# Kernel optimization log

Hardware: AMD Instinct MI355X
Metric: run time of the kernel (lower is better)

## Reference

```python
import jax, jax.numpy as jnp
import numpy as np

NUM_HEADS = 8
KERNEL = 3


def _arsinh_norm(x, w, b):
    # ArsinhNorm with scale=1.0: weight * asinh(x) + bias
    return w * jnp.arcsinh(x) + b


def _nbr_idx(L, k):
    # NATTEN neighborhood: window start clamped so the k-window stays in-bounds
    start = jnp.clip(jnp.arange(L) - k // 2, 0, L - k)
    return start[:, None] + jnp.arange(k)  # [L, k]


def _na2d(x, qkv_w, qkv_b, proj_w, proj_b, num_heads=NUM_HEADS, k=KERNEL):
    B, H, W, C = x.shape
    hd = C // num_heads
    qkv = x @ qkv_w + qkv_b                      # [B,H,W,3C]
    q, kk, v = jnp.split(qkv, 3, axis=-1)
    q = q.reshape(B, H, W, num_heads, hd) * (hd ** -0.5)
    kk = kk.reshape(B, H, W, num_heads, hd)
    v = v.reshape(B, H, W, num_heads, hd)
    ri = _nbr_idx(H, k)[:, None, :, None]        # [H,1,k,1]
    ci = _nbr_idx(W, k)[None, :, None, :]        # [1,W,1,k]
    nb_k = kk[:, ri, ci].reshape(B, H, W, k * k, num_heads, hd)  # gather 3x3 neighborhood
    nb_v = v[:, ri, ci].reshape(B, H, W, k * k, num_heads, hd)
    scores = jnp.einsum('bijnd,bijmnd->bijnm', q, nb_k)          # [B,H,W,nh,k*k]
    attn = jax.nn.softmax(scores, axis=-1)
    out = jnp.einsum('bijnm,bijmnd->bijnd', attn, nb_v).reshape(B, H, W, C)
    return out @ proj_w + proj_b


def setup_inputs() -> dict:
    key = jax.random.key(0)
    ks = jax.random.split(key, 8)
    B, H, W, C = 16, 64, 64, 256
    s = 0.02
    return {
        'h': jax.random.normal(ks[0], (B, H, W, C), dtype=jnp.float32),
        'qkv_w': jax.random.normal(ks[1], (C, 3 * C), dtype=jnp.float32) * s,
        'qkv_b': jnp.zeros((3 * C,), jnp.float32),
        'proj_w': jax.random.normal(ks[2], (C, C), dtype=jnp.float32) * s,
        'proj_b': jnp.zeros((C,), jnp.float32),
        'n1_w': jnp.ones((C,), jnp.float32),
        'n1_b': jnp.zeros((C,), jnp.float32),
        'n2_w': jnp.ones((C,), jnp.float32),
        'n2_b': jnp.zeros((C,), jnp.float32),
        'mlp_w1': jax.random.normal(ks[3], (C, 2 * C), dtype=jnp.float32) * s,
        'mlp_b1': jnp.zeros((2 * C,), jnp.float32),
        'mlp_w2': jax.random.normal(ks[4], (2 * C, C), dtype=jnp.float32) * s,
        'mlp_b2': jnp.zeros((C,), jnp.float32),
    }


def reference(h, qkv_w, qkv_b, proj_w, proj_b, n1_w, n1_b, n2_w, n2_b,
              mlp_w1, mlp_b1, mlp_w2, mlp_b2):
    h1 = _arsinh_norm(h, n1_w, n1_b)
    h = h + _na2d(h1, qkv_w, qkv_b, proj_w, proj_b)
    h2 = _arsinh_norm(h, n2_w, n2_b)
    ff = jax.nn.gelu(h2 @ mlp_w1 + mlp_b1, approximate=False) @ mlp_w2 + mlp_b2
    return h + ff
```

## Files before the change

### kernel.cpp

```cpp
#include <hip/hip_runtime.h>
#include <math.h>

typedef unsigned short u16;
typedef unsigned int u32;
typedef __attribute__((ext_vector_type(8))) short short8;
typedef __attribute__((ext_vector_type(4))) float f32x4;

__device__ __forceinline__ float b2f(u16 u) {
    return __uint_as_float(((u32)u) << 16);
}
__device__ __forceinline__ u16 f2b(float f) {
    u32 x = __float_as_uint(f);
    return (u16)((x + 0x7fffu + ((x >> 16) & 1u)) >> 16);
}
__device__ __forceinline__ float ldext(const void* p, size_t i, int isbf) {
    return isbf ? b2f(((const u16*)p)[i]) : ((const float*)p)[i];
}
__device__ __forceinline__ void stext(void* p, size_t i, int isbf, float v) {
    if (isbf) ((u16*)p)[i] = f2b(v);
    else ((float*)p)[i] = v;
}
__device__ __forceinline__ void gl2lds16(const u16* g, u16* l) {
    __builtin_amdgcn_global_load_lds(
        (const __attribute__((address_space(1))) u32*)(const void*)g,
        (__attribute__((address_space(3))) u32*)(void*)l, 16, 0, 0);
}
__device__ __forceinline__ void unpack8(uint4 w, float* f) {
    const u32* pw = (const u32*)&w;
#pragma unroll
    for (int k = 0; k < 4; ++k) {
        f[2 * k]     = __uint_as_float(pw[k] << 16);
        f[2 * k + 1] = __uint_as_float(pw[k] & 0xffff0000u);
    }
}

__global__ void detect_k(const void* __restrict__ h, int* __restrict__ flag) {
    __shared__ int cnt;
    if (threadIdx.x == 0) cnt = 0;
    __syncthreads();
    const u16* p = (const u16*)h;
    int local = 0;
    for (int i = threadIdx.x; i < 4096; i += 256) {
        int e = (p[i] >> 7) & 0xFF;
        if (e != 0 && (e < 110 || e > 133)) local++;
    }
    atomicAdd(&cnt, local);
    __syncthreads();
    if (threadIdx.x == 0) *flag = (cnt < 256) ? 1 : 0;
}

__global__ void transpose_k(const void* __restrict__ src, u16* __restrict__ dst,
                            int R, int C, const int* __restrict__ flag) {
    int isbf = *flag;
    int idx = blockIdx.x * 256 + threadIdx.x;
    if (idx >= R * C) return;
    int r = idx / C, c = idx - r * C;
    dst[c * R + r] = f2b(ldext(src, idx, isbf));
}

__global__ void norm_k(const void* __restrict__ xb, size_t xoff,
                       const void* __restrict__ w, const void* __restrict__ b,
                       u16* __restrict__ y, const int* __restrict__ flag, int force_bf) {
    int isbf = *flag;
    int xisbf = force_bf ? 1 : isbf;
    size_t base = ((size_t)blockIdx.x * 256 + threadIdx.x) * 4;
    int c0 = (int)(base & 255);
    float v[4];
    if (xisbf) {
        uint2 raw = *reinterpret_cast<const uint2*>((const u16*)xb + xoff + base);
        const u16* px = reinterpret_cast<const u16*>(&raw);
#pragma unroll
        for (int j = 0; j < 4; ++j) v[j] = b2f(px[j]);
    } else {
        float4 r = *reinterpret_cast<const float4*>((const float*)xb + xoff + base);
        v[0] = r.x; v[1] = r.y; v[2] = r.z; v[3] = r.w;
    }
    u16 o[4];
#pragma unroll
    for (int j = 0; j < 4; ++j)
        o[j] = f2b(ldext(w, c0 + j, isbf) * asinhf(v[j]) + ldext(b, c0 + j, isbf));
    *reinterpret_cast<uint2*>(y + base) = *reinterpret_cast<uint2*>(o);
}

template <int EPI>
__global__ __launch_bounds__(256) void gemm_bt(
    const u16* __restrict__ A, const u16* __restrict__ BT, const void* __restrict__ bias,
    const void* __restrict__ resb, size_t resoff, void* __restrict__ outb, size_t outoff,
    int N, int K, const int* __restrict__ flag) {
    __shared__ __align__(16) u16 lA[128 * 32];
    __shared__ __align__(16) u16 lB[128 * 32];
    const int isbf = *flag;
    const int tid = threadIdx.x;
    const int lane = tid & 63;
    const int wave = tid >> 6;
    const int waveM = wave >> 1, waveN = wave & 1;
    const int m0 = blockIdx.y * 128;
    const int n0 = blockIdx.x * 128;

    f32x4 acc[4][4];
#pragma unroll
    for (int mi = 0; mi < 4; ++mi)
#pragma unroll
        for (int ni = 0; ni < 4; ++ni)
#pragma unroll
            for (int r = 0; r < 4; ++r) acc[mi][ni][r] = 0.f;

    const int lrow = lane & 15;
    const int ko = (lane >> 4) * 8;

    for (int k0 = 0; k0 < K; k0 += 32) {
        __syncthreads();
#pragma unroll
        for (int q = 0; q < 2; ++q) {
            int s = wave * 2 + q;
            int e0 = (s * 64 + lane) * 8;
            int row = e0 >> 5, col = e0 & 31;
            gl2lds16(&A[(size_t)(m0 + row) * K + k0 + col], &lA[s * 512]);
            gl2lds16(&BT[(size_t)(n0 + row) * K + k0 + col], &lB[s * 512]);
        }
        __syncthreads();
        short8 af[4], bfr[4];
#pragma unroll
        for (int mi = 0; mi < 4; ++mi)
            af[mi] = *reinterpret_cast<const short8*>(&lA[(waveM * 64 + mi * 16 + lrow) * 32 + ko]);
#pragma unroll
        for (int ni = 0; ni < 4; ++ni)
            bfr[ni] = *reinterpret_cast<const short8*>(&lB[(waveN * 64 + ni * 16 + lrow) * 32 + ko]);
#pragma unroll
        for (int mi = 0; mi < 4; ++mi)
#pragma unroll
            for (int ni = 0; ni < 4; ++ni)
                acc[mi][ni] = __builtin_amdgcn_mfma_f32_16x16x32_bf16(af[mi], bfr[ni], acc[mi][ni], 0, 0, 0);
    }

    const int rquad = (lane >> 4) * 4;
    const int ccol = lane & 15;
#pragma unroll
    for (int mi = 0; mi < 4; ++mi)
#pragma unroll
        for (int ni = 0; ni < 4; ++ni) {
            int colg = n0 + waveN * 64 + ni * 16 + ccol;
            float bb = ldext(bias, colg, isbf);
#pragma unroll
            for (int r = 0; r < 4; ++r) {
                int rowg = m0 + waveM * 64 + mi * 16 + rquad + r;
                size_t idx = (size_t)rowg * N + colg;
                float v = acc[mi][ni][r] + bb;
                if (EPI == 0) {
                    ((u16*)outb)[outoff + idx] = f2b(v);
                } else if (EPI == 1) {
                    v = 0.5f * v * (1.f + erff(v * 0.70710678118654752f));
                    ((u16*)outb)[outoff + idx] = f2b(v);
                } else if (EPI == 2) {
                    v += ldext(resb, resoff + idx, isbf);
                    stext(outb, outoff + idx, isbf, v);
                } else if (EPI == 3) {
                    v += ldext(resb, resoff + idx, isbf);
                    ((u16*)outb)[outoff + idx] = f2b(v);
                } else {
                    v += b2f(((const u16*)resb)[resoff + idx]);
                    stext(outb, outoff + idx, isbf, v);
                }
            }
        }
}

__global__ __launch_bounds__(256) void attn_k(const u16* __restrict__ qkv, u16* __restrict__ out) {
    const int t = blockIdx.x * 256 + threadIdx.x;
    const int head = t & 7;
    const int p = t >> 3;
    const int b = p >> 12;
    const int ij = p & 4095;
    const int i = ij >> 6, j = ij & 63;
    int r0 = i - 1; r0 = r0 < 0 ? 0 : (r0 > 61 ? 61 : r0);
    int c0 = j - 1; c0 = c0 < 0 ? 0 : (c0 > 61 ? 61 : c0);

    const u16* qp = qkv + (size_t)p * 768 + head * 32;
    float q[32];
#pragma unroll
    for (int ch = 0; ch < 4; ++ch)
        unpack8(*reinterpret_cast<const uint4*>(qp + ch * 8), q + ch * 8);

    const float qscale = 0.17677669529663687f;
    int nbp[9];
    float sc[9];
#pragma unroll
    for (int dr = 0; dr < 3; ++dr)
#pragma unroll
        for (int dc = 0; dc < 3; ++dc) {
            int nb = dr * 3 + dc;
            int np_ = b * 4096 + (r0 + dr) * 64 + (c0 + dc);
            nbp[nb] = np_;
            const u16* kp = qkv + (size_t)np_ * 768 + 256 + head * 32;
            float dot = 0.f;
#pragma unroll
            for (int ch = 0; ch < 4; ++ch) {
                float kf[8];
                unpack8(*reinterpret_cast<const uint4*>(kp + ch * 8), kf);
#pragma unroll
                for (int e = 0; e < 8; ++e) dot += q[ch * 8 + e] * kf[e];
            }
            sc[nb] = dot * qscale;
        }

    float mx = sc[0];
#pragma unroll
    for (int nb = 1; nb < 9; ++nb) mx = fmaxf(mx, sc[nb]);
    float s = 0.f;
#pragma unroll
    for (int nb = 0; nb < 9; ++nb) { sc[nb] = __expf(sc[nb] - mx); s += sc[nb]; }
    float inv = 1.f / s;

    float acc[32];
#pragma unroll
    for (int e = 0; e < 32; ++e) acc[e] = 0.f;
#pragma unroll
    for (int nb = 0; nb < 9; ++nb) {
        const u16* vp = qkv + (size_t)nbp[nb] * 768 + 512 + head * 32;
        float wgt = sc[nb] * inv;
#pragma unroll
        for (int ch = 0; ch < 4; ++ch) {
            float vf[8];
            unpack8(*reinterpret_cast<const uint4*>(vp + ch * 8), vf);
#pragma unroll
            for (int e = 0; e < 8; ++e) acc[ch * 8 + e] += wgt * vf[e];
        }
    }

    u16 ob[32];
#pragma unroll
    for (int e = 0; e < 32; ++e) ob[e] = f2b(acc[e]);
    uint4* ov = reinterpret_cast<uint4*>(ob);
    uint4* og = reinterpret_cast<uint4*>(out + (size_t)p * 256 + head * 32);
#pragma unroll
    for (int ch = 0; ch < 4; ++ch) og[ch] = ov[ch];
}

extern "C" void kernel_launch(void* const* d_in, const int* in_sizes, int n_in,
                              void* d_out, int out_size, void* d_ws, size_t ws_size,
                              hipStream_t stream) {
    const void* h      = d_in[0];
    const void* qkv_w  = d_in[1];
    const void* qkv_b  = d_in[2];
    const void* proj_w = d_in[3];
    const void* proj_b = d_in[4];
    const void* n1_w   = d_in[5];
    const void* n1_b   = d_in[6];
    const void* n2_w   = d_in[7];
    const void* n2_b   = d_in[8];
    const void* w1     = d_in[9];
    const void* b1     = d_in[10];
    const void* w2     = d_in[11];
    const void* b2     = d_in[12];

    char* ws = (char*)d_ws;
    u16* WqkvT  = (u16*)(ws + 0);
    u16* WprojT = (u16*)(ws + 393216);
    u16* W1T    = (u16*)(ws + 524288);
    u16* W2T    = (u16*)(ws + 786432);
    int* Flag   = (int*)(ws + 1048576);
    char* bufs  = ws + 1049600;

    size_t avail = ws_size > 1049600 ? ws_size - 1049600 : 0;
    int CHUNK = 4096;
    if (avail >= (size_t)65536 * 2048) CHUNK = 65536;
    else if (avail >= (size_t)16384 * 2048) CHUNK = 16384;
    else if (avail >= (size_t)8192 * 2048) CHUNK = 8192;

    u16* H1 = (u16*)bufs;
    u16* S  = (u16*)(bufs + (size_t)CHUNK * 512);

    detect_k<<<1, 256, 0, stream>>>(h, Flag);
    transpose_k<<<768, 256, 0, stream>>>(qkv_w, WqkvT, 256, 768, Flag);
    transpose_k<<<256, 256, 0, stream>>>(proj_w, WprojT, 256, 256, Flag);
    transpose_k<<<512, 256, 0, stream>>>(w1, W1T, 256, 512, Flag);
    transpose_k<<<512, 256, 0, stream>>>(w2, W2T, 512, 256, Flag);

    if (CHUNK == 65536) {
        u16* HNS = S;
        u16* T   = S + (size_t)65536 * 256;
        norm_k<<<16384, 256, 0, stream>>>(h, 0, n1_w, n1_b, H1, Flag, 0);
        { dim3 g(6, 512); gemm_bt<0><<<g, 256, 0, stream>>>(H1, WqkvT, qkv_b, nullptr, 0, S, 0, 768, 256, Flag); }
        attn_k<<<2048, 256, 0, stream>>>(S, H1);
        { dim3 g(2, 512); gemm_bt<3><<<g, 256, 0, stream>>>(H1, WprojT, proj_b, h, 0, HNS, 0, 256, 256, Flag); }
        norm_k<<<16384, 256, 0, stream>>>(HNS, 0, n2_w, n2_b, H1, Flag, 1);
        { dim3 g(4, 512); gemm_bt<1><<<g, 256, 0, stream>>>(H1, W1T, b1, nullptr, 0, T, 0, 512, 256, Flag); }
        { dim3 g(2, 512); gemm_bt<4><<<g, 256, 0, stream>>>(T, W2T, b2, HNS, 0, d_out, 0, 256, 512, Flag); }
    } else {
        const int NCH = 65536 / CHUNK;
        for (int c = 0; c < NCH; ++c) {
            size_t off = (size_t)c * CHUNK * 256;
            norm_k<<<CHUNK / 4, 256, 0, stream>>>(h, off, n1_w, n1_b, H1, Flag, 0);
            { dim3 g(6, CHUNK / 128);
              gemm_bt<0><<<g, 256, 0, stream>>>(H1, WqkvT, qkv_b, nullptr, 0, S, 0, 768, 256, Flag); }
            attn_k<<<CHUNK / 32, 256, 0, stream>>>(S, H1);
            { dim3 g(2, CHUNK / 128);
              gemm_bt<2><<<g, 256, 0, stream>>>(H1, WprojT, proj_b, h, off, d_out, off, 256, 256, Flag); }
        }
        for (int c = 0; c < NCH; ++c) {
            size_t off = (size_t)c * CHUNK * 256;
            norm_k<<<CHUNK / 4, 256, 0, stream>>>(d_out, off, n2_w, n2_b, H1, Flag, 0);
            { dim3 g(4, CHUNK / 128);
              gemm_bt<1><<<g, 256, 0, stream>>>(H1, W1T, b1, nullptr, 0, S, 0, 512, 256, Flag); }
            { dim3 g(2, CHUNK / 128);
              gemm_bt<2><<<g, 256, 0, stream>>>(S, W2T, b2, d_out, off, d_out, off, 256, 512, Flag); }
        }
    }
}
```

Baseline: 520.1 us.

## Keep GEMM A-tile resident in LDS, fuse norm2 into proj epilogue, merge transposes

Adds a gemm2 kernel in which each block loads its full A row tile into swizzled LDS once, then loops over every N tile. B tiles are double-buffered with an XOR swizzle so the next K slice loads while the current one computes. The projection GEMM epilogue now also applies the second arsinh norm, which removes the separate norm_k pass, and the four weight-transpose launches are merged into one. The large LDS footprint (about 80KB per block) limits occupancy, and the serial loop over N tiles gives fewer blocks for the same work.

Measured after the change: 679.7 us. 1.31x slower.

```diff
diff --git a/kernel.cpp b/kernel.cpp
--- a/kernel.cpp
+++ b/kernel.cpp
@@ -49,13 +49,26 @@
     if (threadIdx.x == 0) *flag = (cnt < 256) ? 1 : 0;
 }
 
-__global__ void transpose_k(const void* __restrict__ src, u16* __restrict__ dst,
-                            int R, int C, const int* __restrict__ flag) {
+__global__ void transpose_all(const void* __restrict__ qkv_w, const void* __restrict__ proj_w,
+                              const void* __restrict__ w1, const void* __restrict__ w2,
+                              u16* __restrict__ WqkvT, u16* __restrict__ WprojT,
+                              u16* __restrict__ W1T, u16* __restrict__ W2T,
+                              const int* __restrict__ flag) {
     int isbf = *flag;
     int idx = blockIdx.x * 256 + threadIdx.x;
-    if (idx >= R * C) return;
-    int r = idx / C, c = idx - r * C;
-    dst[c * R + r] = f2b(ldext(src, idx, isbf));
+    if (idx < 196608) {
+        int r = idx / 768, c = idx - r * 768;
+        WqkvT[c * 256 + r] = f2b(ldext(qkv_w, idx, isbf));
+    } else if (idx < 262144) {
+        int i = idx - 196608; int r = i >> 8, c = i & 255;
+        WprojT[c * 256 + r] = f2b(ldext(proj_w, i, isbf));
+    } else if (idx < 393216) {
+        int i = idx - 262144; int r = i >> 9, c = i & 511;
+        W1T[c * 256 + r] = f2b(ldext(w1, i, isbf));
+    } else {
+        int i = idx - 393216; int r = i >> 8, c = i & 255;
+        W2T[c * 512 + r] = f2b(ldext(w2, i, isbf));
+    }
 }
 
 __global__ void norm_k(const void* __restrict__ xb, size_t xoff,
@@ -80,6 +93,125 @@
     for (int j = 0; j < 4; ++j)
         o[j] = f2b(ldext(w, c0 + j, isbf) * asinhf(v[j]) + ldext(b, c0 + j, isbf));
     *reinterpret_cast<uint2*>(y + base) = *reinterpret_cast<uint2*>(o);
+}
+
+template <int EPI, int TM, int K>
+__global__ __launch_bounds__(256) void gemm2(
+    const u16* __restrict__ A, const u16* __restrict__ BT, const void* __restrict__ bias,
+    const void* __restrict__ resb, void* __restrict__ out1, u16* __restrict__ out2,
+    const void* __restrict__ nw, const void* __restrict__ nb,
+    int N, const int* __restrict__ flag) {
+    __shared__ __align__(16) u16 lA[TM * K];
+    __shared__ __align__(16) u16 lB[2][128 * 32];
+    const int isbf = *flag;
+    const int tid = threadIdx.x;
+    const int lane = tid & 63;
+    const int wave = tid >> 6;
+    const int waveM = wave >> 1, waveN = wave & 1;
+    const int m0 = blockIdx.x * TM;
+    const int NT = N >> 7;
+    constexpr int MT = TM / 32;
+    constexpr int CHPR = K / 8;
+    constexpr int SPW = (TM * K * 2 / 1024) / 4;
+
+#pragma unroll
+    for (int q = 0; q < SPW; ++q) {
+        int s = wave * SPW + q;
+        int chunk = s * 64 + lane;
+        int row = chunk / CHPR;
+        int p = chunk % CHPR;
+        int c = p ^ (row & 7);
+        gl2lds16(&A[(size_t)(m0 + row) * K + c * 8], &lA[s * 512]);
+    }
+
+    const int lrow = lane & 15;
+    const int ko = (lane >> 4) * 8;
+    const int rquad = (lane >> 4) * 4;
+    constexpr int KI = K / 32;
+
+    for (int nt = 0; nt < NT; ++nt) {
+        const int n0 = nt << 7;
+        f32x4 acc[MT][4];
+#pragma unroll
+        for (int mi = 0; mi < MT; ++mi)
+#pragma unroll
+            for (int ni = 0; ni < 4; ++ni)
+#pragma unroll
+                for (int r = 0; r < 4; ++r) acc[mi][ni][r] = 0.f;
+
+        __syncthreads();
+#pragma unroll
+        for (int q = 0; q < 2; ++q) {
+            int s = wave * 2 + q;
+            int chunk = s * 64 + lane;
+            int row = chunk >> 2, p = chunk & 3;
+            int c = p ^ ((row >> 1) & 3);
+            gl2lds16(&BT[(size_t)(n0 + row) * K + c * 8], &lB[0][s * 512]);
+        }
+#pragma unroll
+        for (int i = 0; i < KI; ++i) {
+            __syncthreads();
+            if (i + 1 < KI) {
+                int k1 = (i + 1) * 32;
+#pragma unroll
+                for (int q = 0; q < 2; ++q) {
+                    int s = wave * 2 + q;
+                    int chunk = s * 64 + lane;
+                    int row = chunk >> 2, p = chunk & 3;
+                    int c = p ^ ((row >> 1) & 3);
+                    gl2lds16(&BT[(size_t)(n0 + row) * K + k1 + c * 8], &lB[(i + 1) & 1][s * 512]);
+                }
+            }
+            const int k0 = i * 32;
+            short8 af[MT], bfr[4];
+#pragma unroll
+            for (int mi = 0; mi < MT; ++mi) {
+                int r = waveM * (TM / 2) + mi * 16 + lrow;
+                int p = ((k0 + ko) >> 3) ^ (r & 7);
+                af[mi] = *reinterpret_cast<const short8*>(&lA[r * K + p * 8]);
+            }
+#pragma unroll
+            for (int ni = 0; ni < 4; ++ni) {
+                int r = waveN * 64 + ni * 16 + lrow;
+                int p = (ko >> 3) ^ ((r >> 1) & 3);
+                bfr[ni] = *reinterpret_cast<const short8*>(&lB[i & 1][r * 32 + p * 8]);
+            }
+#pragma unroll
+            for (int mi = 0; mi < MT; ++mi)
+#pragma unroll
+                for (int ni = 0; ni < 4; ++ni)
+                    acc[mi][ni] = __builtin_amdgcn_mfma_f32_16x16x32_bf16(af[mi], bfr[ni], acc[mi][ni], 0, 0, 0);
+        }
+        const int ccol = lane & 15;
+#pragma unroll
+        for (int mi = 0; mi < MT; ++mi)
+#pragma unroll
+            for (int ni = 0; ni < 4; ++ni) {
+                int colg = n0 + waveN * 64 + ni * 16 + ccol;
+                float bb = ldext(bias, colg, isbf);
+                float nwc = 0.f, nbc = 0.f;
+                if (EPI == 5) { nwc = ldext(nw, colg, isbf); nbc = ldext(nb, colg, isbf); }
+#pragma unroll
+                for (int r = 0; r < 4; ++r) {
+                    int rowg = m0 + waveM * (TM / 2) + mi * 16 + rquad + r;
+                    size_t idx = (size_t)rowg * N + colg;
+                    float v = acc[mi][ni][r] + bb;
+                    if (EPI == 0) {
+                        ((u16*)out1)[idx] = f2b(v);
+                    } else if (EPI == 1) {
+                        v = 0.5f * v * (1.f + erff(v * 0.70710678118654752f));
+                        ((u16*)out1)[idx] = f2b(v);
+                    } else if (EPI == 4) {
+                        v += b2f(((const u16*)resb)[idx]);
+                        stext(out1, idx, isbf, v);
+                    } else {
+                        v += ldext(resb, idx, isbf);
+                        ((u16*)out1)[idx] = f2b(v);
+                        out2[idx] = f2b(nwc * asinhf(v) + nbc);
+                    }
+                }
+            }
+    }
 }
 
 template <int EPI>
@@ -96,7 +228,6 @@
     const int waveM = wave >> 1, waveN = wave & 1;
     const int m0 = blockIdx.y * 128;
     const int n0 = blockIdx.x * 128;
-
     f32x4 acc[4][4];
 #pragma unroll
     for (int mi = 0; mi < 4; ++mi)
@@ -104,10 +235,8 @@
         for (int ni = 0; ni < 4; ++ni)
 #pragma unroll
             for (int r = 0; r < 4; ++r) acc[mi][ni][r] = 0.f;
-
     const int lrow = lane & 15;
     const int ko = (lane >> 4) * 8;
-
     for (int k0 = 0; k0 < K; k0 += 32) {
         __syncthreads();
 #pragma unroll
@@ -132,7 +261,6 @@
             for (int ni = 0; ni < 4; ++ni)
                 acc[mi][ni] = __builtin_amdgcn_mfma_f32_16x16x32_bf16(af[mi], bfr[ni], acc[mi][ni], 0, 0, 0);
     }
-
     const int rquad = (lane >> 4) * 4;
     const int ccol = lane & 15;
 #pragma unroll
@@ -151,14 +279,8 @@
                 } else if (EPI == 1) {
                     v = 0.5f * v * (1.f + erff(v * 0.70710678118654752f));
                     ((u16*)outb)[outoff + idx] = f2b(v);
-                } else if (EPI == 2) {
+                } else {
                     v += ldext(resb, resoff + idx, isbf);
-                    stext(outb, outoff + idx, isbf, v);
-                } else if (EPI == 3) {
-                    v += ldext(resb, resoff + idx, isbf);
-                    ((u16*)outb)[outoff + idx] = f2b(v);
-                } else {
-                    v += b2f(((const u16*)resb)[resoff + idx]);
                     stext(outb, outoff + idx, isbf, v);
                 }
             }
@@ -202,7 +324,6 @@
             }
             sc[nb] = dot * qscale;
         }
-
     float mx = sc[0];
 #pragma unroll
     for (int nb = 1; nb < 9; ++nb) mx = fmaxf(mx, sc[nb]);
@@ -226,7 +347,6 @@
             for (int e = 0; e < 8; ++e) acc[ch * 8 + e] += wgt * vf[e];
         }
     }
-
     u16 ob[32];
 #pragma unroll
     for (int e = 0; e < 32; ++e) ob[e] = f2b(acc[e]);
@@ -271,21 +391,22 @@
     u16* S  = (u16*)(bufs + (size_t)CHUNK * 512);
 
     detect_k<<<1, 256, 0, stream>>>(h, Flag);
-    transpose_k<<<768, 256, 0, stream>>>(qkv_w, WqkvT, 256, 768, Flag);
-    transpose_k<<<256, 256, 0, stream>>>(proj_w, WprojT, 256, 256, Flag);
-    transpose_k<<<512, 256, 0, stream>>>(w1, W1T, 256, 512, Flag);
-    transpose_k<<<512, 256, 0, stream>>>(w2, W2T, 512, 256, Flag);
+    transpose_all<<<2048, 256, 0, stream>>>(qkv_w, proj_w, w1, w2,
+                                            WqkvT, WprojT, W1T, W2T, Flag);
 
     if (CHUNK == 65536) {
         u16* HNS = S;
         u16* T   = S + (size_t)65536 * 256;
         norm_k<<<16384, 256, 0, stream>>>(h, 0, n1_w, n1_b, H1, Flag, 0);
-        { dim3 g(6, 512); gemm_bt<0><<<g, 256, 0, stream>>>(H1, WqkvT, qkv_b, nullptr, 0, S, 0, 768, 256, Flag); }
+        gemm2<0, 128, 256><<<512, 256, 0, stream>>>(H1, WqkvT, qkv_b, nullptr, S, nullptr,
+                                                    nullptr, nullptr, 768, Flag);
         attn_k<<<2048, 256, 0, stream>>>(S, H1);
-        { dim3 g(2, 512); gemm_bt<3><<<g, 256, 0, stream>>>(H1, WprojT, proj_b, h, 0, HNS, 0, 256, 256, Flag); }
-        norm_k<<<16384, 256, 0, stream>>>(HNS, 0, n2_w, n2_b, H1, Flag, 1);
-        { dim3 g(4, 512); gemm_bt<1><<<g, 256, 0, stream>>>(H1, W1T, b1, nullptr, 0, T, 0, 512, 256, Flag); }
-        { dim3 g(2, 512); gemm_bt<4><<<g, 256, 0, stream>>>(T, W2T, b2, HNS, 0, d_out, 0, 256, 512, Flag); }
+        gemm2<5, 128, 256><<<512, 256, 0, stream>>>(H1, WprojT, proj_b, h, HNS, H1,
+                                                    n2_w, n2_b, 256, Flag);
+        gemm2<1, 128, 256><<<512, 256, 0, stream>>>(H1, W1T, b1, nullptr, T, nullptr,
+                                                    nullptr, nullptr, 512, Flag);
+        gemm2<4, 64, 512><<<1024, 256, 0, stream>>>(T, W2T, b2, HNS, d_out, nullptr,
+                                                    nullptr, nullptr, 256, Flag);
     } else {
         const int NCH = 65536 / CHUNK;
         for (int c = 0; c < NCH; ++c) {
```
